# Kernel optimization log

Hardware: AMD Instinct MI355X
Metric: run time of the kernel (lower is better)

The kernel has to match this reference:

```python
import jax, jax.numpy as jnp
import numpy as np

B, N, K = 2, 16384, 16
C_IN, C_OUT, SHARE = 64, 64, 8
ATTN = C_OUT // SHARE  # 8
EPS = 1e-5


def bn(x, gamma, beta):
    # BatchNorm2d_P: normalize over (B, N, K) per channel, training-mode batch stats
    m = jnp.mean(x, axis=(0, 1, 2), keepdims=True)
    v = jnp.var(x, axis=(0, 1, 2), keepdims=True)  # biased variance
    return (x - m) * jax.lax.rsqrt(v + EPS) * gamma + beta


def gather(points, idx):
    # points: (B, N, C), idx: (B, N, K) -> (B, N, K, C)
    b, n, k = idx.shape
    flat = idx.reshape(b, n * k)
    out = jnp.take_along_axis(points, flat[:, :, None], axis=1)
    return out.reshape(b, n, k, points.shape[-1])


def setup_inputs() -> dict:
    key = jax.random.key(0)
    ks = jax.random.split(key, 16)
    w = lambda k_, shp: (jax.random.normal(k_, shp, dtype=jnp.float32) * 0.02)
    inp = {
        "xyz": jax.random.normal(ks[0], (B, N, 3), dtype=jnp.float32),
        "features": jax.random.normal(ks[1], (B, N, C_IN), dtype=jnp.float32),
        "knn_idx": jax.random.randint(ks[2], (B, N, K), 0, N),
        "Wq": w(ks[3], (C_IN, C_OUT)), "bq": jnp.zeros((C_OUT,), jnp.float32),
        "Wk": w(ks[4], (C_IN, C_OUT)), "bk": jnp.zeros((C_OUT,), jnp.float32),
        "Wv": w(ks[5], (C_IN, C_OUT)), "bv": jnp.zeros((C_OUT,), jnp.float32),
        "Wd1": w(ks[6], (3, 3)), "bd1": jnp.zeros((3,), jnp.float32),
        "gamma_d": jnp.ones((3,), jnp.float32), "beta_d": jnp.zeros((3,), jnp.float32),
        "Wd2": w(ks[7], (3, C_OUT)), "bd2": jnp.zeros((C_OUT,), jnp.float32),
        "gamma_g1": jnp.ones((C_OUT,), jnp.float32), "beta_g1": jnp.zeros((C_OUT,), jnp.float32),
        "Wg1": w(ks[8], (C_OUT, ATTN)), "bg1": jnp.zeros((ATTN,), jnp.float32),
        "gamma_g2": jnp.ones((ATTN,), jnp.float32), "beta_g2": jnp.zeros((ATTN,), jnp.float32),
        "Wg2": w(ks[9], (ATTN, ATTN)), "bg2": jnp.zeros((ATTN,), jnp.float32),
    }
    return inp


def reference(xyz, features, knn_idx, Wq, bq, Wk, bk, Wv, bv,
              Wd1, bd1, gamma_d, beta_d, Wd2, bd2,
              gamma_g1, beta_g1, Wg1, bg1, gamma_g2, beta_g2, Wg2, bg2):
    q = features @ Wq + bq                       # (B,N,C_OUT)
    k = gather(features @ Wk + bk, knn_idx)      # (B,N,K,C_OUT)
    v = gather(features @ Wv + bv, knn_idx)      # (B,N,K,C_OUT)
    knn_xyz = gather(xyz, knn_idx)               # (B,N,K,3)
    rel = xyz[:, :, None, :] - knn_xyz           # (B,N,K,3)
    # fc_delta: Linear(3,3) -> BN -> ReLU -> Linear(3,C_OUT)
    pos_enc = jax.nn.relu(bn(rel @ Wd1 + bd1, gamma_d, beta_d)) @ Wd2 + bd2  # (B,N,K,C_OUT)
    # einops.reduce 'b n k (i j) -> b n k j' with j=mid_planes is identity (i=1)
    attn_in = q[:, :, None, :] - k + pos_enc     # (B,N,K,C_OUT)
    # fc_gamma: BN -> ReLU -> Linear(C_OUT,ATTN) -> BN -> ReLU -> Linear(ATTN,ATTN)
    h = jax.nn.relu(bn(attn_in, gamma_g1, beta_g1)) @ Wg1 + bg1  # (B,N,K,ATTN)
    h = jax.nn.relu(bn(h, gamma_g2, beta_g2)) @ Wg2 + bg2        # (B,N,K,ATTN)
    attn = jax.nn.softmax(h, axis=2)             # softmax over K neighbors
    vp = (v + pos_enc).reshape(B, N, K, SHARE, ATTN)
    res = jnp.einsum('bnksa,bnka->bnsa', vp, attn)
    return res.reshape(B, N, C_OUT)
```

## Files before the change

### kernel.cpp

```cpp
#include <hip/hip_runtime.h>
#include <hip/hip_bf16.h>
#include <type_traits>

#define BB 2
#define NN 16384
#define KK 16
#define CC 64
#define AA 8
#define BN_PTS (BB*NN)
#define TOT (BB*NN*KK)
#define EPS 1e-5f

using bf = __hip_bfloat16;

__device__ __forceinline__ float b2f(bf x) { return __bfloat162float(x); }

__device__ __forceinline__ unsigned short f2bu(float x) {
    bf b = __float2bfloat16(x);
    unsigned short u;
    __builtin_memcpy(&u, &b, 2);
    return u;
}
__device__ __forceinline__ unsigned packbf(float lo, float hi) {
    return (unsigned)f2bu(lo) | ((unsigned)f2bu(hi) << 16);
}

template<typename T> __device__ __forceinline__ float ldt(const void* p, int i) {
    if constexpr (std::is_same<T, bf>::value) return b2f(((const bf*)p)[i]);
    else return ((const float*)p)[i];
}
template<typename T> __device__ __forceinline__ void stt(void* p, int i, float v) {
    if constexpr (std::is_same<T, bf>::value) ((bf*)p)[i] = __float2bfloat16(v);
    else ((float*)p)[i] = v;
}

__device__ __forceinline__ float waveReduce(float v) {
    #pragma unroll
    for (int off = 32; off; off >>= 1) v += __shfl_down(v, off, 64);
    return v;
}

__device__ __forceinline__ bool probe_bf(const unsigned* gbits) {
    return gbits[0] == 0x3F803F80u;
}

template<typename T>
__device__ void qkv_body(float* smem,
    const void* feat, const void* Wq, const void* bq, const void* Wk, const void* bk,
    const void* Wv, const void* bv, float* qf, bf* kfb, bf* vfb)
{
    float* fs = smem;
    const int t = threadIdx.x;
    const int which = t >> 6;
    const int c = t & 63;
    const int row0 = blockIdx.x * 32;

    for (int i = t; i < 32*64; i += 256)
        fs[i] = ldt<T>(feat, row0*64 + i);

    float w[64];
    float bb_ = 0.f;
    const void* W    = (which == 0) ? Wq : (which == 1) ? Wk : Wv;
    const void* bias = (which == 0) ? bq : (which == 1) ? bk : bv;
    if (which < 3) {
        #pragma unroll
        for (int j = 0; j < 64; j++) w[j] = ldt<T>(W, j*64 + c);
        bb_ = ldt<T>(bias, c);
    }
    __syncthreads();

    if (which < 3) {
        for (int r = 0; r < 32; r++) {
            float acc = bb_;
            #pragma unroll
            for (int j = 0; j < 64; j++) acc = fmaf(fs[r*64 + j], w[j], acc);
            const int idx = (row0 + r)*64 + c;
            if (which == 0)      qf[idx]  = acc;
            else if (which == 1) kfb[idx] = __float2bfloat16(acc);
            else                 vfb[idx] = __float2bfloat16(acc);
        }
    }
}

template<typename T>
__device__ void statsd_body(float* smem,
    const void* xyz, const int* knn, const void* Wd1, const void* bd1,
    float* part, float* dx, float* dy, float* dz)
{
    float w[9], bi[3];
    #pragma unroll
    for (int i = 0; i < 9; i++) w[i] = ldt<T>(Wd1, i);
    #pragma unroll
    for (int i = 0; i < 3; i++) bi[i] = ldt<T>(bd1, i);

    const int sb = blockIdx.x - 1024;
    float s[6] = {0,0,0,0,0,0};
    #pragma unroll
    for (int u = 0; u < 4; u++) {
        const int p = sb*1024 + u*256 + threadIdx.x;
        const int bn = p >> 4;
        const int b  = bn >> 14;
        const int j  = knn[p];
        const int nb = (b << 14) + j;
        const float r0 = ldt<T>(xyz, bn*3+0) - ldt<T>(xyz, nb*3+0);
        const float r1 = ldt<T>(xyz, bn*3+1) - ldt<T>(xyz, nb*3+1);
        const float r2 = ldt<T>(xyz, bn*3+2) - ldt<T>(xyz, nb*3+2);
        const float d0 = fmaf(r0, w[0], fmaf(r1, w[3], fmaf(r2, w[6], bi[0])));
        const float d1 = fmaf(r0, w[1], fmaf(r1, w[4], fmaf(r2, w[7], bi[1])));
        const float d2 = fmaf(r0, w[2], fmaf(r1, w[5], fmaf(r2, w[8], bi[2])));
        if (dx) { dx[p] = d0; dy[p] = d1; dz[p] = d2; }
        s[0] += d0; s[1] += d1; s[2] += d2;
        s[3] = fmaf(d0, d0, s[3]); s[4] = fmaf(d1, d1, s[4]); s[5] = fmaf(d2, d2, s[5]);
    }
    float* red = smem;
    const int lane = threadIdx.x & 63, wave = threadIdx.x >> 6;
    #pragma unroll
    for (int i = 0; i < 6; i++) {
        const float r = waveReduce(s[i]);
        if (lane == 0) red[wave*6 + i] = r;
    }
    __syncthreads();
    if (threadIdx.x < 6)
        part[sb*8 + threadIdx.x] =
            red[threadIdx.x] + red[6+threadIdx.x] + red[12+threadIdx.x] + red[18+threadIdx.x];
}

__global__ __launch_bounds__(256) void qkv_statsd_kernel(
    const unsigned* __restrict__ gbits,
    const void* feat, const void* Wq, const void* bq, const void* Wk, const void* bk,
    const void* Wv, const void* bv,
    const void* xyz, const int* __restrict__ knn, const void* Wd1, const void* bd1,
    float* qf, bf* kfb, bf* vfb,
    float* part, float* dx, float* dy, float* dz)
{
    extern __shared__ float smem[];
    const bool isbf = probe_bf(gbits);
    if (blockIdx.x < 1024) {
        if (isbf) qkv_body<bf>(smem, feat, Wq, bq, Wk, bk, Wv, bv, qf, kfb, vfb);
        else      qkv_body<float>(smem, feat, Wq, bq, Wk, bk, Wv, bv, qf, kfb, vfb);
    } else {
        if (isbf) statsd_body<bf>(smem, xyz, knn, Wd1, bd1, part, dx, dy, dz);
        else      statsd_body<float>(smem, xyz, knn, Wd1, bd1, part, dx, dy, dz);
    }
}

template<typename T>
__device__ void finalize_d_body(float* smem,
    const float* part, const void* gamma, const void* beta, float* coef)
{
    float* red  = smem;
    float* sums = smem + 256;
    const int t = threadIdx.x;
    const int col = t & 7, chunk = t >> 3;
    float s = 0.f;
    for (int r = chunk; r < 512; r += 32) s += part[r*8 + col];
    red[chunk*8 + col] = s;
    __syncthreads();
    if (t < 8) {
        float a = 0.f;
        #pragma unroll
        for (int c = 0; c < 32; c++) a += red[c*8 + t];
        sums[t] = a;
    }
    __syncthreads();
    if (t < 3) {
        const float mean = sums[t] / (float)TOT;
        const float var  = sums[3+t] / (float)TOT - mean*mean;
        const float sc   = ldt<T>(gamma, t) * rsqrtf(var + EPS);
        coef[t]   = sc;
        coef[4+t] = ldt<T>(beta, t) - mean*sc;
    }
}
__global__ __launch_bounds__(256) void finalize_d(const unsigned* __restrict__ gbits,
    const float* __restrict__ part, const void* gamma, const void* beta, float* coef)
{
    extern __shared__ float smem[];
    if (probe_bf(gbits)) finalize_d_body<bf>(smem, part, gamma, beta, coef);
    else                 finalize_d_body<float>(smem, part, gamma, beta, coef);
}

template<typename T>
__device__ void statsg1_body(float* smem,
    const void* xyz, const int* knn, const float* qf, const bf* kfb,
    const void* Wd1, const void* bd1, const void* Wd2, const void* bd2,
    const float* coefd, float* part,
    const float* dx, const float* dy, const float* dz, bf* aibuf)
{
    const int lane = threadIdx.x & 63, wave = threadIdx.x >> 6;
    float w1[9], b1[3], sc[3], sh[3];
    #pragma unroll
    for (int i = 0; i < 9; i++) w1[i] = ldt<T>(Wd1, i);
    #pragma unroll
    for (int i = 0; i < 3; i++) { b1[i] = ldt<T>(bd1, i); sc[i] = coefd[i]; sh[i] = coefd[4+i]; }
    const float w2a = ldt<T>(Wd2, lane), w2b = ldt<T>(Wd2, 64+lane), w2c = ldt<T>(Wd2, 128+lane);
    const float bd2c = ldt<T>(bd2, lane);

    float sum = 0.f, sq = 0.f;
    for (int bn = blockIdx.x*4 + wave; bn < BN_PTS; bn += 2048*4) {
        const int b = bn >> 14;
        const float qv = qf[bn*64 + lane];
        float x0 = 0.f, x1 = 0.f, x2 = 0.f;
        if (!dx) { x0 = ldt<T>(xyz, bn*3+0); x1 = ldt<T>(xyz, bn*3+1); x2 = ldt<T>(xyz, bn*3+2); }
        #pragma unroll
        for (int k = 0; k < 16; k++) {
            const int it = bn*16 + k;
            const int j  = knn[it];
            const int nb = (b << 14) + j;
            float d0, d1, d2;
            if (dx) {
                d0 = dx[it]; d1 = dy[it]; d2 = dz[it];
            } else {
                const float r0 = x0 - ldt<T>(xyz, nb*3+0);
                const float r1 = x1 - ldt<T>(xyz, nb*3+1);
                const float r2 = x2 - ldt<T>(xyz, nb*3+2);
                d0 = fmaf(r0, w1[0], fmaf(r1, w1[3], fmaf(r2, w1[6], b1[0])));
                d1 = fmaf(r0, w1[1], fmaf(r1, w1[4], fmaf(r2, w1[7], b1[1])));
                d2 = fmaf(r0, w1[2], fmaf(r1, w1[5], fmaf(r2, w1[8], b1[2])));
            }
            d0 = fmaxf(fmaf(d0, sc[0], sh[0]), 0.f);
            d1 = fmaxf(fmaf(d1, sc[1], sh[1]), 0.f);
            d2 = fmaxf(fmaf(d2, sc[2], sh[2]), 0.f);
            const float pos = fmaf(d0, w2a, fmaf(d1, w2b, fmaf(d2, w2c, bd2c)));
            const float at = qv - b2f(kfb[nb*64 + lane]) + pos;
            if (aibuf) aibuf[(size_t)it*64 + lane] = __float2bfloat16(at);
            sum += at; sq = fmaf(at, at, sq);
        }
    }
    float* ls = smem;
    float* lq = smem + 256;
    ls[wave*64 + lane] = sum; lq[wave*64 + lane] = sq;
    __syncthreads();
    if (threadIdx.x < 64) {
        float a = 0.f, q = 0.f;
        #pragma unroll
        for (int w = 0; w < 4; w++) { a += ls[w*64 + lane]; q += lq[w*64 + lane]; }
        part[blockIdx.x*128 + lane]      = a;
        part[blockIdx.x*128 + 64 + lane] = q;
    }
}
__global__ __launch_bounds__(256) void statsg1_kernel(
    const unsigned* __restrict__ gbits,
    const void* xyz, const int* __restrict__ knn, const float* __restrict__ qf,
    const bf* __restrict__ kfb,
    const void* Wd1, const void* bd1, const void* Wd2, const void* bd2,
    const float* __restrict__ coefd, float* part,
    const float* dx, const float* dy, const float* dz, bf* aibuf)
{
    extern __shared__ float smem[];
    if (probe_bf(gbits)) statsg1_body<bf>(smem, xyz, knn, qf, kfb, Wd1, bd1, Wd2, bd2, coefd, part, dx, dy, dz, aibuf);
    else                 statsg1_body<float>(smem, xyz, knn, qf, kfb, Wd1, bd1, Wd2, bd2, coefd, part, dx, dy, dz, aibuf);
}

__global__ __launch_bounds__(256) void reduce_g1(const float* __restrict__ part,
                                                 float* __restrict__ partB)
{
    __shared__ float red[2][128];
    const int t = threadIdx.x;
    const int col = t & 127, chunk = t >> 7;
    const int r0 = blockIdx.x * 32;
    float s = 0.f;
    #pragma unroll
    for (int j = 0; j < 16; j++) s += part[(r0 + chunk + 2*j)*128 + col];
    red[chunk][col] = s;
    __syncthreads();
    if (t < 128) partB[blockIdx.x*128 + t] = red[0][t] + red[1][t];
}

template<typename T>
__device__ void finalize_g1_body(float* smem,
    const float* partB, const void* gamma, const void* beta, float* coef)
{
    float* red  = smem;
    float* sums = smem + 512;
    const int t = threadIdx.x;
    const int col = t & 127, chunk = t >> 7;
    float s = 0.f;
    #pragma unroll
    for (int j = 0; j < 16; j++) s += partB[(chunk + 4*j)*128 + col];
    red[chunk*128 + col] = s;
    __syncthreads();
    if (t < 128) sums[t] = red[t] + red[128+t] + red[256+t] + red[384+t];
    __syncthreads();
    if (t < 64) {
        const float mean = sums[t] / (float)TOT;
        const float var  = sums[64+t] / (float)TOT - mean*mean;
        const float sc   = ldt<T>(gamma, t) * rsqrtf(var + EPS);
        coef[t]    = sc;
        coef[64+t] = ldt<T>(beta, t) - mean*sc;
    }
}
__global__ __launch_bounds__(512) void finalize_g1(const unsigned* __restrict__ gbits,
    const float* __restrict__ partB, const void* gamma, const void* beta, float* coef)
{
    extern __shared__ float smem[];
    if (probe_bf(gbits)) finalize_g1_body<bf>(smem, partB, gamma, beta, coef);
    else                 finalize_g1_body<float>(smem, partB, gamma, beta, coef);
}

template<typename T>
__device__ void h1_fast_body(float* smem,
    const unsigned* aibuf, const float* coefg1, const void* Wg1, const void* bg1,
    unsigned* h1b, float* part)
{
    float* wg1s = smem;
    float* scs  = smem + 512;
    float* shs  = smem + 576;
    float* ssum = smem + 640;
    float* ssq  = smem + 672;
    const int t = threadIdx.x, lane = t & 63, wave = t >> 6;
    for (int i = t; i < 512; i += 256) wg1s[i] = ldt<T>(Wg1, i);
    if (t < 64) { scs[t] = coefg1[t]; shs[t] = coefg1[64 + t]; }
    __syncthreads();

    const size_t item = (size_t)blockIdx.x*256 + t;
    const uint4* src = (const uint4*)aibuf + item*8;
    float h[8];
    #pragma unroll
    for (int a = 0; a < 8; a++) h[a] = ldt<T>(bg1, a);
    #pragma unroll
    for (int cb = 0; cb < 8; cb++) {
        const uint4 u = src[cb];
        const unsigned uu[4] = {u.x, u.y, u.z, u.w};
        #pragma unroll
        for (int q = 0; q < 4; q++) {
            const int c0 = cb*8 + q*2;
            const float xlo = __uint_as_float(uu[q] << 16);
            const float xhi = __uint_as_float(uu[q] & 0xffff0000u);
            const float g0 = fmaxf(fmaf(xlo, scs[c0],   shs[c0]),   0.f);
            const float g1 = fmaxf(fmaf(xhi, scs[c0+1], shs[c0+1]), 0.f);
            #pragma unroll
            for (int a = 0; a < 8; a++) {
                h[a] = fmaf(g0, wg1s[c0*8 + a], h[a]);
                h[a] = fmaf(g1, wg1s[(c0+1)*8 + a], h[a]);
            }
        }
    }
    uint4 o4;
    o4.x = packbf(h[0], h[1]); o4.y = packbf(h[2], h[3]);
    o4.z = packbf(h[4], h[5]); o4.w = packbf(h[6], h[7]);
    ((uint4*)h1b)[item] = o4;

    #pragma unroll
    for (int a = 0; a < 8; a++) {
        const float rs = waveReduce(h[a]);
        const float rq = waveReduce(h[a]*h[a]);
        if (lane == 0) { ssum[wave*8 + a] = rs; ssq[wave*8 + a] = rq; }
    }
    __syncthreads();
    if (t < 8) {
        part[blockIdx.x*16 + t]     = ssum[t] + ssum[8+t] + ssum[16+t] + ssum[24+t];
        part[blockIdx.x*16 + 8 + t] = ssq[t]  + ssq[8+t]  + ssq[16+t]  + ssq[24+t];
    }
}
__global__ __launch_bounds__(256) void h1_fast(const unsigned* __restrict__ gbits,
    const unsigned* __restrict__ aibuf, const float* __restrict__ coefg1,
    const void* Wg1, const void* bg1, unsigned* h1b, float* part)
{
    extern __shared__ float smem[];
    if (probe_bf(gbits)) h1_fast_body<bf>(smem, aibuf, coefg1, Wg1, bg1, h1b, part);
    else                 h1_fast_body<float>(smem, aibuf, coefg1, Wg1, bg1, h1b, part);
}

#define H1_PAD 68
template<typename T>
__device__ void h1_body(float* smem,
    const void* xyz, const int* knn, const float* qf, const bf* kfb,
    const void* Wd1, const void* bd1, const void* Wd2, const void* bd2,
    const float* coefd, const float* coefg1, const void* Wg1, const void* bg1,
    unsigned* h1b, float* part)
{
    float* xs   = smem;
    float* wg1s = smem + 8704;
    float* ssum = smem + 9216;
    float* ssq  = smem + 9248;
    const int t = threadIdx.x;
    const int lane = t & 63, wave = t >> 6;

    for (int i = t; i < 512; i += 256) wg1s[i] = ldt<T>(Wg1, i);

    float w1[9], b1[3], scd[3], shd[3];
    #pragma unroll
    for (int i = 0; i < 9; i++) w1[i] = ldt<T>(Wd1, i);
    #pragma unroll
    for (int i = 0; i < 3; i++) { b1[i] = ldt<T>(bd1, i); scd[i] = coefd[i]; shd[i] = coefd[4+i]; }
    const float w2a = ldt<T>(Wd2, lane), w2b = ldt<T>(Wd2, 64+lane), w2c = ldt<T>(Wd2, 128+lane);
    const float bd2c = ldt<T>(bd2, lane);
    const float sc1 = coefg1[lane], sh1 = coefg1[64+lane];
    const int lslot = (lane < 32) ? lane : lane + 4;

    #pragma unroll
    for (int g = 0; g < 2; g++) {
        const int pl = wave*2 + g;
        const int bn = blockIdx.x*8 + pl;
        const int b  = bn >> 14;
        const float qv = qf[bn*64 + lane];
        const float x0 = ldt<T>(xyz, bn*3+0), x1 = ldt<T>(xyz, bn*3+1), x2 = ldt<T>(xyz, bn*3+2);
        #pragma unroll
        for (int k = 0; k < 16; k++) {
            const int j  = knn[bn*16 + k];
            const int nb = (b << 14) + j;
            const float r0 = x0 - ldt<T>(xyz, nb*3+0);
            const float r1 = x1 - ldt<T>(xyz, nb*3+1);
            const float r2 = x2 - ldt<T>(xyz, nb*3+2);
            float d0 = fmaf(r0, w1[0], fmaf(r1, w1[3], fmaf(r2, w1[6], b1[0])));
            float d1 = fmaf(r0, w1[1], fmaf(r1, w1[4], fmaf(r2, w1[7], b1[1])));
            float d2 = fmaf(r0, w1[2], fmaf(r1, w1[5], fmaf(r2, w1[8], b1[2])));
            d0 = fmaxf(fmaf(d0, scd[0], shd[0]), 0.f);
            d1 = fmaxf(fmaf(d1, scd[1], shd[1]), 0.f);
            d2 = fmaxf(fmaf(d2, scd[2], shd[2]), 0.f);
            const float pos = fmaf(d0, w2a, fmaf(d1, w2b, fmaf(d2, w2c, bd2c)));
            const float at = qv - b2f(kfb[nb*64 + lane]) + pos;
            xs[(pl*16 + k)*H1_PAD + lslot] = fmaxf(fmaf(at, sc1, sh1), 0.f);
        }
    }
    __syncthreads();

    const int item = t >> 1;
    const int half = t & 1;
    float h[8];
    #pragma unroll
    for (int a = 0; a < 8; a++) h[a] = half ? 0.f : ldt<T>(bg1, a);
    const float4* xr = (const float4*)(xs + item*H1_PAD + half*36);
    const float* wbase = wg1s + half*256;
    #pragma unroll
    for (int cb = 0; cb < 8; cb++) {
        const float4 xv = xr[cb];
        #pragma unroll
        for (int jj = 0; jj < 4; jj++) {
            const float x = (jj == 0) ? xv.x : (jj == 1) ? xv.y : (jj == 2) ? xv.z : xv.w;
            const float4 wa = *(const float4*)&wbase[(cb*4 + jj)*8];
            const float4 wb = *(const float4*)&wbase[(cb*4 + jj)*8 + 4];
            h[0] = fmaf(x, wa.x, h[0]); h[1] = fmaf(x, wa.y, h[1]);
            h[2] = fmaf(x, wa.z, h[2]); h[3] = fmaf(x, wa.w, h[3]);
            h[4] = fmaf(x, wb.x, h[4]); h[5] = fmaf(x, wb.y, h[5]);
            h[6] = fmaf(x, wb.z, h[6]); h[7] = fmaf(x, wb.w, h[7]);
        }
    }
    #pragma unroll
    for (int a = 0; a < 8; a++) h[a] += __shfl_xor(h[a], 1, 64);

    const int it = blockIdx.x*128 + item;
    if (half == 0) {
        uint4 o4;
        o4.x = packbf(h[0], h[1]); o4.y = packbf(h[2], h[3]);
        o4.z = packbf(h[4], h[5]); o4.w = packbf(h[6], h[7]);
        ((uint4*)h1b)[it] = o4;
    }
    #pragma unroll
    for (int a = 0; a < 8; a++) {
        const float rs = waveReduce(h[a]);
        const float rq = waveReduce(h[a]*h[a]);
        if (lane == 0) { ssum[wave*8 + a] = 0.5f*rs; ssq[wave*8 + a] = 0.5f*rq; }
    }
    __syncthreads();
    if (t < 8) {
        part[blockIdx.x*16 + t]     = ssum[t] + ssum[8+t] + ssum[16+t] + ssum[24+t];
        part[blockIdx.x*16 + 8 + t] = ssq[t]  + ssq[8+t]  + ssq[16+t]  + ssq[24+t];
    }
}
__global__ __launch_bounds__(256, 4) void h1_kernel(const unsigned* __restrict__ gbits,
    const void* xyz, const int* __restrict__ knn, const float* __restrict__ qf,
    const bf* __restrict__ kfb,
    const void* Wd1, const void* bd1, const void* Wd2, const void* bd2,
    const float* __restrict__ coefd, const float* __restrict__ coefg1,
    const void* Wg1, const void* bg1, unsigned* h1b, float* part)
{
    extern __shared__ float smem[];
    if (probe_bf(gbits)) h1_body<bf>(smem, xyz, knn, qf, kfb, Wd1, bd1, Wd2, bd2, coefd, coefg1, Wg1, bg1, h1b, part);
    else                 h1_body<float>(smem, xyz, knn, qf, kfb, Wd1, bd1, Wd2, bd2, coefd, coefg1, Wg1, bg1, h1b, part);
}

__global__ __launch_bounds__(256) void reduce_g2(const float* __restrict__ part,
                                                 float* __restrict__ partB, int rows)
{
    __shared__ float red[16][16];
    const int t = threadIdx.x;
    const int col = t & 15, chunk = t >> 4;
    const int rpb = rows >> 6;
    const int r0 = blockIdx.x * rpb;
    float s = 0.f;
    for (int r = chunk; r < rpb; r += 16) s += part[(r0 + r)*16 + col];
    red[chunk][col] = s;
    __syncthreads();
    if (t < 16) {
        float a = 0.f;
        #pragma unroll
        for (int c = 0; c < 16; c++) a += red[c][t];
        partB[blockIdx.x*16 + t] = a;
    }
}

template<typename T>
__device__ void finalize_g2_body(float* smem,
    const float* partB, const void* gamma, const void* beta, float* coef)
{
    float* red  = smem;
    float* sums = smem + 256;
    const int t = threadIdx.x;
    const int col = t & 15, chunk = t >> 4;
    float s = 0.f;
    #pragma unroll
    for (int j = 0; j < 4; j++) s += partB[(chunk + 16*j)*16 + col];
    red[chunk*16 + col] = s;
    __syncthreads();
    if (t < 16) {
        float a = 0.f;
        #pragma unroll
        for (int c = 0; c < 16; c++) a += red[c*16 + t];
        sums[t] = a;
    }
    __syncthreads();
    if (t < 8) {
        const float mean = sums[t] / (float)TOT;
        const float var  = sums[8+t] / (float)TOT - mean*mean;
        const float sc   = ldt<T>(gamma, t) * rsqrtf(var + EPS);
        coef[t]   = sc;
        coef[8+t] = ldt<T>(beta, t) - mean*sc;
    }
}
__global__ __launch_bounds__(256) void finalize_g2(const unsigned* __restrict__ gbits,
    const float* __restrict__ partB, const void* gamma, const void* beta, float* coef)
{
    extern __shared__ float smem[];
    if (probe_bf(gbits)) finalize_g2_body<bf>(smem, partB, gamma, beta, coef);
    else                 finalize_g2_body<float>(smem, partB, gamma, beta, coef);
}

template<typename T>
__device__ void out_body(float* smem,
    const void* xyz, const int* knn, const bf* vfb, const unsigned* h1b,
    const void* Wd1, const void* bd1, const void* Wd2, const void* bd2,
    const float* coefd, const float* coefg2, const void* Wg2, const void* bg2,
    const float* dx, const float* dy, const float* dz, void* out)
{
    float* g   = smem;
    float* hh  = smem + 2048;
    float* dd  = smem + 4096;
    float* wg2 = smem + 4864;
    float* s3  = smem + 4928;
    int*  idxs = (int*)(smem + 5312);
    const int t = threadIdx.x;
    const int bn0 = blockIdx.x * 16;

    if (t < 64) wg2[t] = ldt<T>(Wg2, t);

    {
        const int p = t >> 4, q = t & 15;
        const uint4 u = ((const uint4*)h1b)[(size_t)(bn0 + p)*16 + q];
        const unsigned uu[4] = {u.x, u.y, u.z, u.w};
        #pragma unroll
        for (int w = 0; w < 4; w++) {
            const int c0 = q*8 + w*2;
            const int a = c0 & 7;
            const float xlo = __uint_as_float(uu[w] << 16);
            const float xhi = __uint_as_float(uu[w] & 0xffff0000u);
            g[p*128 + c0]     = fmaxf(fmaf(xlo, coefg2[a],   coefg2[8+a]),   0.f);
            g[p*128 + c0 + 1] = fmaxf(fmaf(xhi, coefg2[a+1], coefg2[9+a]),   0.f);
        }
    }
    {
        const int p = t >> 4, k = t & 15;
        const int bn = bn0 + p;
        const int b = bn >> 14;
        const int it = bn*16 + k;
        const int j = knn[it];
        idxs[p*16 + k] = j;
        float d0, d1, d2;
        if (dx) {
            d0 = dx[it]; d1 = dy[it]; d2 = dz[it];
        } else {
            const int nb = (b << 14) + j;
            const float r0 = ldt<T>(xyz, bn*3+0) - ldt<T>(xyz, nb*3+0);
            const float r1 = ldt<T>(xyz, bn*3+1) - ldt<T>(xyz, nb*3+1);
            const float r2 = ldt<T>(xyz, bn*3+2) - ldt<T>(xyz, nb*3+2);
            d0 = fmaf(r0, ldt<T>(Wd1,0), fmaf(r1, ldt<T>(Wd1,3), fmaf(r2, ldt<T>(Wd1,6), ldt<T>(bd1,0))));
            d1 = fmaf(r0, ldt<T>(Wd1,1), fmaf(r1, ldt<T>(Wd1,4), fmaf(r2, ldt<T>(Wd1,7), ldt<T>(bd1,1))));
            d2 = fmaf(r0, ldt<T>(Wd1,2), fmaf(r1, ldt<T>(Wd1,5), fmaf(r2, ldt<T>(Wd1,8), ldt<T>(bd1,2))));
        }
        dd[(p*16 + k)*3 + 0] = fmaxf(fmaf(d0, coefd[0], coefd[4]), 0.f);
        dd[(p*16 + k)*3 + 1] = fmaxf(fmaf(d1, coefd[1], coefd[5]), 0.f);
        dd[(p*16 + k)*3 + 2] = fmaxf(fmaf(d2, coefd[2], coefd[6]), 0.f);
    }
    __syncthreads();

    {
        #pragma unroll
        for (int i = 0; i < 8; i++) {
            const int o = i*256 + t;
            const int p = o >> 7, f = o & 127;
            const int a = f & 7, k = f >> 3;
            float acc = ldt<T>(bg2, a);
            #pragma unroll
            for (int jj = 0; jj < 8; jj++) acc = fmaf(g[p*128 + k*8 + jj], wg2[jj*8 + a], acc);
            hh[p*128 + f] = acc;
        }
    }
    __syncthreads();

    if (t < 128) {
        const int p = t >> 3, a = t & 7;
        float m = -1e30f;
        #pragma unroll
        for (int k = 0; k < 16; k++) m = fmaxf(m, hh[p*128 + k*8 + a]);
        float e[16]; float s = 0.f;
        #pragma unroll
        for (int k = 0; k < 16; k++) { e[k] = __expf(hh[p*128 + k*8 + a] - m); s += e[k]; }
        const float inv = 1.f / s;
        float a0 = 0.f, a1 = 0.f, a2 = 0.f;
        #pragma unroll
        for (int k = 0; k < 16; k++) {
            const float w_ = e[k] * inv;
            hh[p*128 + k*8 + a] = w_;
            a0 = fmaf(w_, dd[(p*16+k)*3+0], a0);
            a1 = fmaf(w_, dd[(p*16+k)*3+1], a1);
            a2 = fmaf(w_, dd[(p*16+k)*3+2], a2);
        }
        s3[(p*8+a)*3+0] = a0; s3[(p*8+a)*3+1] = a1; s3[(p*8+a)*3+2] = a2;
    }
    __syncthreads();

    {
        #pragma unroll
        for (int i = 0; i < 4; i++) {
            const int o = i*256 + t;
            const int p = o >> 6, c = o & 63, a = c & 7;
            const int bn = bn0 + p;
            const int b = bn >> 14;
            const float w0 = ldt<T>(Wd2, c), w1 = ldt<T>(Wd2, 64 + c), w2 = ldt<T>(Wd2, 128 + c);
            const float bd2c = ldt<T>(bd2, c);
            const int sb = (p*8 + a)*3;
            float acc = fmaf(s3[sb], w0, fmaf(s3[sb+1], w1, fmaf(s3[sb+2], w2, bd2c)));
            #pragma unroll
            for (int k = 0; k < 16; k++) {
                const int j = idxs[p*16 + k];
                acc = fmaf(b2f(vfb[((b << 14) + j)*64 + c]), hh[p*128 + k*8 + a], acc);
            }
            stt<T>(out, bn*64 + c, acc);
        }
    }
}
__global__ __launch_bounds__(256) void out_kernel(const unsigned* __restrict__ gbits,
    const void* xyz, const int* __restrict__ knn, const bf* __restrict__ vfb,
    const unsigned* __restrict__ h1b,
    const void* Wd1, const void* bd1, const void* Wd2, const void* bd2,
    const float* __restrict__ coefd, const float* __restrict__ coefg2,
    const void* Wg2, const void* bg2,
    const float* dx, const float* dy, const float* dz, void* out)
{
    extern __shared__ float smem[];
    if (probe_bf(gbits)) out_body<bf>(smem, xyz, knn, vfb, h1b, Wd1, bd1, Wd2, bd2, coefd, coefg2, Wg2, bg2, dx, dy, dz, out);
    else                 out_body<float>(smem, xyz, knn, vfb, h1b, Wd1, bd1, Wd2, bd2, coefd, coefg2, Wg2, bg2, dx, dy, dz, out);
}

#define WS_BIG_FLOATS 25178272ull

extern "C" void kernel_launch(void* const* d_in, const int* in_sizes, int n_in,
                              void* d_out, int out_size, void* d_ws, size_t ws_size,
                              hipStream_t stream) {
    float* ws = (float*)d_ws;
    const void* xyz  = d_in[0];
    const void* feat = d_in[1];
    const int*  knn  = (const int*)d_in[2];
    const void *Wq = d_in[3], *bq = d_in[4], *Wk = d_in[5], *bk = d_in[6];
    const void *Wv = d_in[7], *bv = d_in[8], *Wd1 = d_in[9], *bd1 = d_in[10];
    const void *gd = d_in[11], *betad = d_in[12], *Wd2 = d_in[13], *bd2 = d_in[14];
    const void *gg1 = d_in[15], *bg1b = d_in[16], *Wg1 = d_in[17], *bg1 = d_in[18];
    const void *gg2 = d_in[19], *bg2b = d_in[20], *Wg2 = d_in[21], *bg2 = d_in[22];
    const unsigned* gbits = (const unsigned*)d_in[11];

    float*    qf      = ws;
    bf*       kfb     = (bf*)(ws + 2097152);
    bf*       vfb     = (bf*)(ws + 3145728);
    unsigned* h1b     = (unsigned*)(ws + 4194304);
    float*    part_d  = ws + 6291456;
    float*    partA   = ws + 6295552;
    float*    partB   = ws + 6819840;
    float*    coef_d  = ws + 6828032;
    float*    coef_g1 = ws + 6828040;
    float*    coef_g2 = ws + 6828168;
    const bool big = ws_size >= WS_BIG_FLOATS * 4ull;
    float* dx    = big ? ws + 6828192 : nullptr;
    float* dy    = big ? ws + 7352480 : nullptr;
    float* dz    = big ? ws + 7876768 : nullptr;
    bf*    aibuf = big ? (bf*)(ws + 8401056) : nullptr;

    qkv_statsd_kernel<<<1536, 256, 8192, stream>>>(gbits, feat, Wq, bq, Wk, bk, Wv, bv,
                                                   xyz, knn, Wd1, bd1,
                                                   qf, kfb, vfb, part_d, dx, dy, dz);
    finalize_d<<<1, 256, 1056, stream>>>(gbits, part_d, gd, betad, coef_d);
    statsg1_kernel<<<2048, 256, 2048, stream>>>(gbits, xyz, knn, qf, kfb, Wd1, bd1, Wd2, bd2,
                                                coef_d, partA, dx, dy, dz, aibuf);
    reduce_g1<<<64, 256, 0, stream>>>(partA, partB);
    finalize_g1<<<1, 512, 2560, stream>>>(gbits, partB, gg1, bg1b, coef_g1);
    if (big) {
        h1_fast<<<2048, 256, 2816, stream>>>(gbits, (const unsigned*)aibuf, coef_g1,
                                             Wg1, bg1, h1b, partA);
        reduce_g2<<<64, 256, 0, stream>>>(partA, partB, 2048);
    } else {
        h1_kernel<<<4096, 256, 37120, stream>>>(gbits, xyz, knn, qf, kfb, Wd1, bd1, Wd2, bd2,
                                                coef_d, coef_g1, Wg1, bg1, h1b, partA);
        reduce_g2<<<64, 256, 0, stream>>>(partA, partB, 4096);
    }
    finalize_g2<<<1, 256, 1088, stream>>>(gbits, partB, gg2, bg2b, coef_g2);
    out_kernel<<<2048, 256, 22272, stream>>>(gbits, xyz, knn, vfb, h1b, Wd1, bd1, Wd2, bd2,
                                             coef_d, coef_g2, Wg2, bg2, dx, dy, dz, d_out);
}
```

Baseline: 247.3 us.

## Replace staged BN-stat reduction kernels with atomic accumulators and in-kernel finalize

Swaps the per-block partial-sum arrays and the separate reduce/finalize kernels for the three batchnorms for atomicAdd into 8-way striped global accumulators. Each consumer kernel now computes mean, variance and scale/shift directly from those accumulators. This drops five small serial launches (finalize_d, reduce_g1, finalize_g1, reduce_g2, finalize_g2) and their launch gaps, at the cost of one memset plus atomic contention. Summation order is now nondeterministic, and every block redundantly recomputes the coefficients.

Result: slower. 271.1 us (+9.6%).

```diff
diff --git a/kernel.cpp b/kernel.cpp
--- a/kernel.cpp
+++ b/kernel.cpp
@@ -43,6 +43,11 @@
 __device__ __forceinline__ bool probe_bf(const unsigned* gbits) {
     return gbits[0] == 0x3F803F80u;
 }
+
+#define ACCD_OFF  0
+#define ACCG1_OFF 64
+#define ACCG2_OFF 1088
+#define ACC_FLOATS 1216
 
 template<typename T>
 __device__ void qkv_body(float* smem,
@@ -85,7 +90,7 @@
 template<typename T>
 __device__ void statsd_body(float* smem,
     const void* xyz, const int* knn, const void* Wd1, const void* bd1,
-    float* part, float* dx, float* dy, float* dz)
+    float* accd, float* dx, float* dy, float* dz)
 {
     float w[9], bi[3];
     #pragma unroll
@@ -121,8 +126,8 @@
     }
     __syncthreads();
     if (threadIdx.x < 6)
-        part[sb*8 + threadIdx.x] =
-            red[threadIdx.x] + red[6+threadIdx.x] + red[12+threadIdx.x] + red[18+threadIdx.x];
+        atomicAdd(&accd[(sb & 7)*8 + threadIdx.x],
+                  red[threadIdx.x] + red[6+threadIdx.x] + red[12+threadIdx.x] + red[18+threadIdx.x]);
 }
 
 __global__ __launch_bounds__(256) void qkv_statsd_kernel(
@@ -131,7 +136,7 @@
     const void* Wv, const void* bv,
     const void* xyz, const int* __restrict__ knn, const void* Wd1, const void* bd1,
     float* qf, bf* kfb, bf* vfb,
-    float* part, float* dx, float* dy, float* dz)
+    float* accd, float* dx, float* dy, float* dz)
 {
     extern __shared__ float smem[];
     const bool isbf = probe_bf(gbits);
@@ -139,51 +144,33 @@
         if (isbf) qkv_body<bf>(smem, feat, Wq, bq, Wk, bk, Wv, bv, qf, kfb, vfb);
         else      qkv_body<float>(smem, feat, Wq, bq, Wk, bk, Wv, bv, qf, kfb, vfb);
     } else {
-        if (isbf) statsd_body<bf>(smem, xyz, knn, Wd1, bd1, part, dx, dy, dz);
-        else      statsd_body<float>(smem, xyz, knn, Wd1, bd1, part, dx, dy, dz);
+        if (isbf) statsd_body<bf>(smem, xyz, knn, Wd1, bd1, accd, dx, dy, dz);
+        else      statsd_body<float>(smem, xyz, knn, Wd1, bd1, accd, dx, dy, dz);
     }
 }
 
 template<typename T>
-__device__ void finalize_d_body(float* smem,
-    const float* part, const void* gamma, const void* beta, float* coef)
-{
-    float* red  = smem;
-    float* sums = smem + 256;
-    const int t = threadIdx.x;
-    const int col = t & 7, chunk = t >> 3;
-    float s = 0.f;
-    for (int r = chunk; r < 512; r += 32) s += part[r*8 + col];
-    red[chunk*8 + col] = s;
-    __syncthreads();
-    if (t < 8) {
-        float a = 0.f;
-        #pragma unroll
-        for (int c = 0; c < 32; c++) a += red[c*8 + t];
-        sums[t] = a;
-    }
-    __syncthreads();
-    if (t < 3) {
-        const float mean = sums[t] / (float)TOT;
-        const float var  = sums[3+t] / (float)TOT - mean*mean;
-        const float sc   = ldt<T>(gamma, t) * rsqrtf(var + EPS);
-        coef[t]   = sc;
-        coef[4+t] = ldt<T>(beta, t) - mean*sc;
-    }
-}
-__global__ __launch_bounds__(256) void finalize_d(const unsigned* __restrict__ gbits,
-    const float* __restrict__ part, const void* gamma, const void* beta, float* coef)
-{
-    extern __shared__ float smem[];
-    if (probe_bf(gbits)) finalize_d_body<bf>(smem, part, gamma, beta, coef);
-    else                 finalize_d_body<float>(smem, part, gamma, beta, coef);
+__device__ __forceinline__ void coefd_from_acc(const float* accd,
+    const void* gd, const void* betad, float* sc, float* sh)
+{
+    #pragma unroll
+    for (int i = 0; i < 3; i++) {
+        float s = 0.f, q = 0.f;
+        #pragma unroll
+        for (int c = 0; c < 8; c++) { s += accd[c*8 + i]; q += accd[c*8 + 3 + i]; }
+        const float mean = s / (float)TOT;
+        const float var  = q / (float)TOT - mean*mean;
+        sc[i] = ldt<T>(gd, i) * rsqrtf(var + EPS);
+        sh[i] = ldt<T>(betad, i) - mean*sc[i];
+    }
 }
 
 template<typename T>
 __device__ void statsg1_body(float* smem,
     const void* xyz, const int* knn, const float* qf, const bf* kfb,
     const void* Wd1, const void* bd1, const void* Wd2, const void* bd2,
-    const float* coefd, float* part,
+    const void* gd, const void* betad,
+    const float* accd, float* accg1,
     const float* dx, const float* dy, const float* dz, bf* aibuf)
 {
     const int lane = threadIdx.x & 63, wave = threadIdx.x >> 6;
@@ -191,7 +178,8 @@
     #pragma unroll
     for (int i = 0; i < 9; i++) w1[i] = ldt<T>(Wd1, i);
     #pragma unroll
-    for (int i = 0; i < 3; i++) { b1[i] = ldt<T>(bd1, i); sc[i] = coefd[i]; sh[i] = coefd[4+i]; }
+    for (int i = 0; i < 3; i++) b1[i] = ldt<T>(bd1, i);
+    coefd_from_acc<T>(accd, gd, betad, sc, sh);
     const float w2a = ldt<T>(Wd2, lane), w2b = ldt<T>(Wd2, 64+lane), w2c = ldt<T>(Wd2, 128+lane);
     const float bd2c = ldt<T>(bd2, lane);
 
@@ -234,8 +222,9 @@
         float a = 0.f, q = 0.f;
         #pragma unroll
         for (int w = 0; w < 4; w++) { a += ls[w*64 + lane]; q += lq[w*64 + lane]; }
-        part[blockIdx.x*128 + lane]      = a;
-        part[blockIdx.x*128 + 64 + lane] = q;
+        const int cp = (blockIdx.x & 7) * 128;
+        atomicAdd(&accg1[cp + lane], a);
+        atomicAdd(&accg1[cp + 64 + lane], q);
     }
 }
 __global__ __launch_bounds__(256) void statsg1_kernel(
@@ -243,64 +232,20 @@
     const void* xyz, const int* __restrict__ knn, const float* __restrict__ qf,
     const bf* __restrict__ kfb,
     const void* Wd1, const void* bd1, const void* Wd2, const void* bd2,
-    const float* __restrict__ coefd, float* part,
+    const void* gd, const void* betad,
+    const float* __restrict__ accd, float* accg1,
     const float* dx, const float* dy, const float* dz, bf* aibuf)
 {
     extern __shared__ float smem[];
-    if (probe_bf(gbits)) statsg1_body<bf>(smem, xyz, knn, qf, kfb, Wd1, bd1, Wd2, bd2, coefd, part, dx, dy, dz, aibuf);
-    else                 statsg1_body<float>(smem, xyz, knn, qf, kfb, Wd1, bd1, Wd2, bd2, coefd, part, dx, dy, dz, aibuf);
-}
-
-__global__ __launch_bounds__(256) void reduce_g1(const float* __restrict__ part,
-                                                 float* __restrict__ partB)
-{
-    __shared__ float red[2][128];
-    const int t = threadIdx.x;
-    const int col = t & 127, chunk = t >> 7;
-    const int r0 = blockIdx.x * 32;
-    float s = 0.f;
-    #pragma unroll
-    for (int j = 0; j < 16; j++) s += part[(r0 + chunk + 2*j)*128 + col];
-    red[chunk][col] = s;
-    __syncthreads();
-    if (t < 128) partB[blockIdx.x*128 + t] = red[0][t] + red[1][t];
-}
-
-template<typename T>
-__device__ void finalize_g1_body(float* smem,
-    const float* partB, const void* gamma, const void* beta, float* coef)
-{
-    float* red  = smem;
-    float* sums = smem + 512;
-    const int t = threadIdx.x;
-    const int col = t & 127, chunk = t >> 7;
-    float s = 0.f;
-    #pragma unroll
-    for (int j = 0; j < 16; j++) s += partB[(chunk + 4*j)*128 + col];
-    red[chunk*128 + col] = s;
-    __syncthreads();
-    if (t < 128) sums[t] = red[t] + red[128+t] + red[256+t] + red[384+t];
-    __syncthreads();
-    if (t < 64) {
-        const float mean = sums[t] / (float)TOT;
-        const float var  = sums[64+t] / (float)TOT - mean*mean;
-        const float sc   = ldt<T>(gamma, t) * rsqrtf(var + EPS);
-        coef[t]    = sc;
-        coef[64+t] = ldt<T>(beta, t) - mean*sc;
-    }
-}
-__global__ __launch_bounds__(512) void finalize_g1(const unsigned* __restrict__ gbits,
-    const float* __restrict__ partB, const void* gamma, const void* beta, float* coef)
-{
-    extern __shared__ float smem[];
-    if (probe_bf(gbits)) finalize_g1_body<bf>(smem, partB, gamma, beta, coef);
-    else                 finalize_g1_body<float>(smem, partB, gamma, beta, coef);
+    if (probe_bf(gbits)) statsg1_body<bf>(smem, xyz, knn, qf, kfb, Wd1, bd1, Wd2, bd2, gd, betad, accd, accg1, dx, dy, dz, aibuf);
+    else                 statsg1_body<float>(smem, xyz, knn, qf, kfb, Wd1, bd1, Wd2, bd2, gd, betad, accd, accg1, dx, dy, dz, aibuf);
 }
 
 template<typename T>
 __device__ void h1_fast_body(float* smem,
-    const unsigned* aibuf, const float* coefg1, const void* Wg1, const void* bg1,
-    unsigned* h1b, float* part)
+    const unsigned* aibuf, const float* accg1,
+    const void* gg1, const void* bg1b, const void* Wg1, const void* bg1,
+    unsigned* h1b, float* accg2)
 {
     float* wg1s = smem;
     float* scs  = smem + 512;
@@ -309,7 +254,16 @@
     float* ssq  = smem + 672;
     const int t = threadIdx.x, lane = t & 63, wave = t >> 6;
     for (int i = t; i < 512; i += 256) wg1s[i] = ldt<T>(Wg1, i);
-    if (t < 64) { scs[t] = coefg1[t]; shs[t] = coefg1[64 + t]; }
+    if (t < 64) {
+        float s = 0.f, q = 0.f;
+        #pragma unroll
+        for (int c = 0; c < 8; c++) { s += accg1[c*128 + t]; q += accg1[c*128 + 64 + t]; }
+        const float mean = s / (float)TOT;
+        const float var  = q / (float)TOT - mean*mean;
+        const float sc   = ldt<T>(gg1, t) * rsqrtf(var + EPS);
+        scs[t] = sc;
+        shs[t] = ldt<T>(bg1b, t) - mean*sc;
+    }
     __syncthreads();
 
     const size_t item = (size_t)blockIdx.x*256 + t;
@@ -348,17 +302,19 @@
     }
     __syncthreads();
     if (t < 8) {
-        part[blockIdx.x*16 + t]     = ssum[t] + ssum[8+t] + ssum[16+t] + ssum[24+t];
-        part[blockIdx.x*16 + 8 + t] = ssq[t]  + ssq[8+t]  + ssq[16+t]  + ssq[24+t];
+        const int cp = (blockIdx.x & 7) * 16;
+        atomicAdd(&accg2[cp + t],     ssum[t] + ssum[8+t] + ssum[16+t] + ssum[24+t]);
+        atomicAdd(&accg2[cp + 8 + t], ssq[t]  + ssq[8+t]  + ssq[16+t]  + ssq[24+t]);
     }
 }
 __global__ __launch_bounds__(256) void h1_fast(const unsigned* __restrict__ gbits,
-    const unsigned* __restrict__ aibuf, const float* __restrict__ coefg1,
-    const void* Wg1, const void* bg1, unsigned* h1b, float* part)
+    const unsigned* __restrict__ aibuf, const float* __restrict__ accg1,
+    const void* gg1, const void* bg1b, const void* Wg1, const void* bg1,
+    unsigned* h1b, float* accg2)
 {
     extern __shared__ float smem[];
-    if (probe_bf(gbits)) h1_fast_body<bf>(smem, aibuf, coefg1, Wg1, bg1, h1b, part);
-    else                 h1_fast_body<float>(smem, aibuf, coefg1, Wg1, bg1, h1b, part);
+    if (probe_bf(gbits)) h1_fast_body<bf>(smem, aibuf, accg1, gg1, bg1b, Wg1, bg1, h1b, accg2);
+    else                 h1_fast_body<float>(smem, aibuf, accg1, gg1, bg1b, Wg1, bg1, h1b, accg2);
 }
 
 #define H1_PAD 68
@@ -366,8 +322,9 @@
 __device__ void h1_body(float* smem,
     const void* xyz, const int* knn, const float* qf, const bf* kfb,
     const void* Wd1, const void* bd1, const void* Wd2, const void* bd2,
-    const float* coefd, const float* coefg1, const void* Wg1, const void* bg1,
-    unsigned* h1b, float* part)
+    const void* gd, const void* betad, const void* gg1, const void* bg1b,
+    const float* accd, const float* accg1,
+    const void* Wg1, const void* bg1, unsigned* h1b, float* accg2)
 {
     float* xs   = smem;
     float* wg1s = smem + 8704;
@@ -382,10 +339,20 @@
     #pragma unroll
     for (int i = 0; i < 9; i++) w1[i] = ldt<T>(Wd1, i);
     #pragma unroll
-    for (int i = 0; i < 3; i++) { b1[i] = ldt<T>(bd1, i); scd[i] = coefd[i]; shd[i] = coefd[4+i]; }
+    for (int i = 0; i < 3; i++) b1[i] = ldt<T>(bd1, i);
+    coefd_from_acc<T>(accd, gd, betad, scd, shd);
     const float w2a = ldt<T>(Wd2, lane), w2b = ldt<T>(Wd2, 64+lane), w2c = ldt<T>(Wd2, 128+lane);
     const float bd2c = ldt<T>(bd2, lane);
-    const float sc1 = coefg1[lane], sh1 = coefg1[64+lane];
+    float sc1, sh1;
+    {
+        float s = 0.f, q = 0.f;
+        #pragma unroll
+        for (int c = 0; c < 8; c++) { s += accg1[c*128 + lane]; q += accg1[c*128 + 64 + lane]; }
+        const float mean = s / (float)TOT;
+        const float var  = q / (float)TOT - mean*mean;
+        sc1 = ldt<T>(gg1, lane) * rsqrtf(var + EPS);
+        sh1 = ldt<T>(bg1b, lane) - mean*sc1;
+    }
     const int lslot = (lane < 32) ? lane : lane + 4;
 
     #pragma unroll
@@ -454,83 +421,31 @@
     }
     __syncthreads();
     if (t < 8) {
-        part[blockIdx.x*16 + t]     = ssum[t] + ssum[8+t] + ssum[16+t] + ssum[24+t];
-        part[blockIdx.x*16 + 8 + t] = ssq[t]  + ssq[8+t]  + ssq[16+t]  + ssq[24+t];
+        const int cp = (blockIdx.x & 7) * 16;
+        atomicAdd(&accg2[cp + t],     ssum[t] + ssum[8+t] + ssum[16+t] + ssum[24+t]);
+        atomicAdd(&accg2[cp + 8 + t], ssq[t]  + ssq[8+t]  + ssq[16+t]  + ssq[24+t]);
     }
 }
 __global__ __launch_bounds__(256, 4) void h1_kernel(const unsigned* __restrict__ gbits,
     const void* xyz, const int* __restrict__ knn, const float* __restrict__ qf,
     const bf* __restrict__ kfb,
     const void* Wd1, const void* bd1, const void* Wd2, const void* bd2,
-    const float* __restrict__ coefd, const float* __restrict__ coefg1,
-    const void* Wg1, const void* bg1, unsigned* h1b, float* part)
+    const void* gd, const void* betad, const void* gg1, const void* bg1b,
+    const float* __restrict__ accd, const float* __restrict__ accg1,
+    const void* Wg1, const void* bg1, unsigned* h1b, float* accg2)
 {
     extern __shared__ float smem[];
-    if (probe_bf(gbits)) h1_body<bf>(smem, xyz, knn, qf, kfb, Wd1, bd1, Wd2, bd2, coefd, coefg1, Wg1, bg1, h1b, part);
-    else                 h1_body<float>(smem, xyz, knn, qf, kfb, Wd1, bd1, Wd2, bd2, coefd, coefg1, Wg1, bg1, h1b, part);
-}
-
-__global__ __launch_bounds__(256) void reduce_g2(const float* __restrict__ part,
-                                                 float* __restrict__ partB, int rows)
-{
-    __shared__ float red[16][16];
-    const int t = threadIdx.x;
-    const int col = t & 15, chunk = t >> 4;
-    const int rpb = rows >> 6;
-    const int r0 = blockIdx.x * rpb;
-    float s = 0.f;
-    for (int r = chunk; r < rpb; r += 16) s += part[(r0 + r)*16 + col];
-    red[chunk][col] = s;
-    __syncthreads();
-    if (t < 16) {
-        float a = 0.f;
-        #pragma unroll
-        for (int c = 0; c < 16; c++) a += red[c][t];
-        partB[blockIdx.x*16 + t] = a;
-    }
-}
-
-template<typename T>
-__device__ void finalize_g2_body(float* smem,
-    const float* partB, const void* gamma, const void* beta, float* coef)
-{
-    float* red  = smem;
-    float* sums = smem + 256;
-    const int t = threadIdx.x;
-    const int col = t & 15, chunk = t >> 4;
-    float s = 0.f;
-    #pragma unroll
-    for (int j = 0; j < 4; j++) s += partB[(chunk + 16*j)*16 + col];
-    red[chunk*16 + col] = s;
-    __syncthreads();
-    if (t < 16) {
-        float a = 0.f;
-        #pragma unroll
-        for (int c = 0; c < 16; c++) a += red[c*16 + t];
-        sums[t] = a;
-    }
-    __syncthreads();
-    if (t < 8) {
-        const float mean = sums[t] / (float)TOT;
-        const float var  = sums[8+t] / (float)TOT - mean*mean;
-        const float sc   = ldt<T>(gamma, t) * rsqrtf(var + EPS);
-        coef[t]   = sc;
-        coef[8+t] = ldt<T>(beta, t) - mean*sc;
-    }
-}
-__global__ __launch_bounds__(256) void finalize_g2(const unsigned* __restrict__ gbits,
-    const float* __restrict__ partB, const void* gamma, const void* beta, float* coef)
-{
-    extern __shared__ float smem[];
-    if (probe_bf(gbits)) finalize_g2_body<bf>(smem, partB, gamma, beta, coef);
-    else                 finalize_g2_body<float>(smem, partB, gamma, beta, coef);
+    if (probe_bf(gbits)) h1_body<bf>(smem, xyz, knn, qf, kfb, Wd1, bd1, Wd2, bd2, gd, betad, gg1, bg1b, accd, accg1, Wg1, bg1, h1b, accg2);
+    else                 h1_body<float>(smem, xyz, knn, qf, kfb, Wd1, bd1, Wd2, bd2, gd, betad, gg1, bg1b, accd, accg1, Wg1, bg1, h1b, accg2);
 }
 
 template<typename T>
 __device__ void out_body(float* smem,
     const void* xyz, const int* knn, const bf* vfb, const unsigned* h1b,
     const void* Wd1, const void* bd1, const void* Wd2, const void* bd2,
-    const float* coefd, const float* coefg2, const void* Wg2, const void* bg2,
+    const void* gd, const void* betad, const void* gg2, const void* bg2b,
+    const float* accd, const float* accg2,
+    const void* Wg2, const void* bg2,
     const float* dx, const float* dy, const float* dz, void* out)
 {
     float* g   = smem;
@@ -539,10 +454,23 @@
     float* wg2 = smem + 4864;
     float* s3  = smem + 4928;
     int*  idxs = (int*)(smem + 5312);
+    float* cg2 = smem + 5568;
     const int t = threadIdx.x;
     const int bn0 = blockIdx.x * 16;
 
     if (t < 64) wg2[t] = ldt<T>(Wg2, t);
+    if (t >= 64 && t < 72) {
+        const int a = t - 64;
+        float s = 0.f, q = 0.f;
+        #pragma unroll
+        for (int c = 0; c < 8; c++) { s += accg2[c*16 + a]; q += accg2[c*16 + 8 + a]; }
+        const float mean = s / (float)TOT;
+        const float var  = q / (float)TOT - mean*mean;
+        const float sc   = ldt<T>(gg2, a) * rsqrtf(var + EPS);
+        cg2[a]     = sc;
+        cg2[8 + a] = ldt<T>(bg2b, a) - mean*sc;
+    }
+    __syncthreads();
 
     {
         const int p = t >> 4, q = t & 15;
@@ -554,11 +482,13 @@
             const int a = c0 & 7;
             const float xlo = __uint_as_float(uu[w] << 16);
             const float xhi = __uint_as_float(uu[w] & 0xffff0000u);
-            g[p*128 + c0]     = fmaxf(fmaf(xlo, coefg2[a],   coefg2[8+a]),   0.f);
-            g[p*128 + c0 + 1] = fmaxf(fmaf(xhi, coefg2[a+1], coefg2[9+a]),   0.f);
+            g[p*128 + c0]     = fmaxf(fmaf(xlo, cg2[a],   cg2[8+a]), 0.f);
+            g[p*128 + c0 + 1] = fmaxf(fmaf(xhi, cg2[a+1], cg2[9+a]), 0.f);
         }
     }
     {
+        float scd[3], shd[3];
+        coefd_from_acc<T>(accd, gd, betad, scd, shd);
         const int p = t >> 4, k = t & 15;
         const int bn = bn0 + p;
         const int b = bn >> 14;
@@ -577,9 +507,9 @@
             d1 = fmaf(r0, ldt<T>(Wd1,1), fmaf(r1, ldt<T>(Wd1,4), fmaf(r2, ldt<T>(Wd1,7), ldt<T>(bd1,1))));
             d2 = fmaf(r0, ldt<T>(Wd1,2), fmaf(r1, ldt<T>(Wd1,5), fmaf(r2, ldt<T>(Wd1,8), ldt<T>(bd1,2))));
         }
-        dd[(p*16 + k)*3 + 0] = fmaxf(fmaf(d0, coefd[0], coefd[4]), 0.f);
-        dd[(p*16 + k)*3 + 1] = fmaxf(fmaf(d1, coefd[1], coefd[5]), 0.f);
-        dd[(p*16 + k)*3 + 2] = fmaxf(fmaf(d2, coefd[2], coefd[6]), 0.f);
+        dd[(p*16 + k)*3 + 0] = fmaxf(fmaf(d0, scd[0], shd[0]), 0.f);
+        dd[(p*16 + k)*3 + 1] = fmaxf(fmaf(d1, scd[1], shd[1]), 0.f);
+        dd[(p*16 + k)*3 + 2] = fmaxf(fmaf(d2, scd[2], shd[2]), 0.f);
     }
     __syncthreads();
 
@@ -643,16 +573,17 @@
     const void* xyz, const int* __restrict__ knn, const bf* __restrict__ vfb,
     const unsigned* __restrict__ h1b,
     const void* Wd1, const void* bd1, const void* Wd2, const void* bd2,
-    const float* __restrict__ coefd, const float* __restrict__ coefg2,
+    const void* gd, const void* betad, const void* gg2, const void* bg2b,
+    const float* __restrict__ accd, const float* __restrict__ accg2,
     const void* Wg2, const void* bg2,
     const float* dx, const float* dy, const float* dz, void* out)
 {
     extern __shared__ float smem[];
-    if (probe_bf(gbits)) out_body<bf>(smem, xyz, knn, vfb, h1b, Wd1, bd1, Wd2, bd2, coefd, coefg2, Wg2, bg2, dx, dy, dz, out);
-    else                 out_body<float>(smem, xyz, knn, vfb, h1b, Wd1, bd1, Wd2, bd2, coefd, coefg2, Wg2, bg2, dx, dy, dz, out);
-}
-
-#define WS_BIG_FLOATS 25178272ull
+    if (probe_bf(gbits)) out_body<bf>(smem, xyz, knn, vfb, h1b, Wd1, bd1, Wd2, bd2, gd, betad, gg2, bg2b, accd, accg2, Wg2, bg2, dx, dy, dz, out);
+    else                 out_body<float>(smem, xyz, knn, vfb, h1b, Wd1, bd1, Wd2, bd2, gd, betad, gg2, bg2b, accd, accg2, Wg2, bg2, dx, dy, dz, out);
+}
+
+#define WS_BIG_FLOATS 24642752ull
 
 extern "C" void kernel_launch(void* const* d_in, const int* in_sizes, int n_in,
                               void* d_out, int out_size, void* d_ws, size_t ws_size,
@@ -668,40 +599,36 @@
     const void *gg2 = d_in[19], *bg2b = d_in[20], *Wg2 = d_in[21], *bg2 = d_in[22];
     const unsigned* gbits = (const unsigned*)d_in[11];
 
-    float*    qf      = ws;
-    bf*       kfb     = (bf*)(ws + 2097152);
-    bf*       vfb     = (bf*)(ws + 3145728);
-    unsigned* h1b     = (unsigned*)(ws + 4194304);
-    float*    part_d  = ws + 6291456;
-    float*    partA   = ws + 6295552;
-    float*    partB   = ws + 6819840;
-    float*    coef_d  = ws + 6828032;
-    float*    coef_g1 = ws + 6828040;
-    float*    coef_g2 = ws + 6828168;
+    float*    qf   = ws;
+    bf*       kfb  = (bf*)(ws + 2097152);
+    bf*       vfb  = (bf*)(ws + 3145728);
+    unsigned* h1b  = (unsigned*)(ws + 4194304);
+    float*    acc  = ws + 6291456;
+    float*    accd  = acc + ACCD_OFF;
+    float*    accg1 = acc + ACCG1_OFF;
+    float*    accg2 = acc + ACCG2_OFF;
     const bool big = ws_size >= WS_BIG_FLOATS * 4ull;
-    float* dx    = big ? ws + 6828192 : nullptr;
-    float* dy    = big ? ws + 7352480 : nullptr;
-    float* dz    = big ? ws + 7876768 : nullptr;
-    bf*    aibuf = big ? (bf*)(ws + 8401056) : nullptr;
+    float* dx    = big ? ws + 6292672 : nullptr;
+    float* dy    = big ? ws + 6816960 : nullptr;
+    float* dz    = big ? ws + 7341248 : nullptr;
+    bf*    aibuf = big ? (bf*)(ws + 7865536) : nullptr;
+
+    hipMemsetAsync(acc, 0, ACC_FLOATS * sizeof(float), stream);
 
     qkv_statsd_kernel<<<1536, 256, 8192, stream>>>(gbits, feat, Wq, bq, Wk, bk, Wv, bv,
                                                    xyz, knn, Wd1, bd1,
-                                                   qf, kfb, vfb, part_d, dx, dy, dz);
-    finalize_d<<<1, 256, 1056, stream>>>(gbits, part_d, gd, betad, coef_d);
+                                                   qf, kfb, vfb, accd, dx, dy, dz);
     statsg1_kernel<<<2048, 256, 2048, stream>>>(gbits, xyz, knn, qf, kfb, Wd1, bd1, Wd2, bd2,
-                                                coef_d, partA, dx, dy, dz, aibuf);
-    reduce_g1<<<64, 256, 0, stream>>>(partA, partB);
-    finalize_g1<<<1, 512, 2560, stream>>>(gbits, partB, gg1, bg1b, coef_g1);
+                                                gd, betad, accd, accg1, dx, dy, dz, aibuf);
     if (big) {
-        h1_fast<<<2048, 256, 2816, stream>>>(gbits, (const unsigned*)aibuf, coef_g1,
-                                             Wg1, bg1, h1b, partA);
-        reduce_g2<<<64, 256, 0, stream>>>(partA, partB, 2048);
+        h1_fast<<<2048, 256, 2816, stream>>>(gbits, (const unsigned*)aibuf, accg1,
+                                             gg1, bg1b, Wg1, bg1, h1b, accg2);
     } else {
         h1_kernel<<<4096, 256, 37120, stream>>>(gbits, xyz, knn, qf, kfb, Wd1, bd1, Wd2, bd2,
-                                                coef_d, coef_g1, Wg1, bg1, h1b, partA);
-        reduce_g2<<<64, 256, 0, stream>>>(partA, partB, 4096);
-    }
-    finalize_g2<<<1, 256, 1088, stream>>>(gbits, partB, gg2, bg2b, coef_g2);
-    out_kernel<<<2048, 256, 22272, stream>>>(gbits, xyz, knn, vfb, h1b, Wd1, bd1, Wd2, bd2,
-                                             coef_d, coef_g2, Wg2, bg2, dx, dy, dz, d_out);
-}
+                                                gd, betad, gg1, bg1b, accd, accg1,
+                                                Wg1, bg1, h1b, accg2);
+    }
+    out_kernel<<<2048, 256, 22336, stream>>>(gbits, xyz, knn, vfb, h1b, Wd1, bd1, Wd2, bd2,
+                                             gd, betad, gg2, bg2b, accd, accg2,
+                                             Wg2, bg2, dx, dy, dz, d_out);
+}
```
